# Kernel tuning notes

Hardware: AMD Instinct MI355X
Metric: run time of the kernel (lower is better)

## Reference

```python
import jax, jax.numpy as jnp
import numpy as np

D = 4096      # hidden_size
H = 32        # num_attention_heads
DH = 128      # head_dim
DR = 64       # rope_head_dim (rotated suffix of head_dim)
G = 4         # o_groups
QLR = 1536    # q_lora_rank
OLR = 512     # o_lora_rank
WIN = 2048    # window_size
EPS = 1e-6    # norm_eps
THETA = 10000.0


def rms_norm(x, g):
    return x * jax.lax.rsqrt(jnp.mean(x * x, axis=-1, keepdims=True) + EPS) * g


def rope_interleave(x, cos, sin):
    # interleaved (non-neox) rotary: pairs are adjacent even/odd lanes
    x0, x1 = x[..., 0::2], x[..., 1::2]
    r0 = x0 * cos - x1 * sin
    r1 = x0 * sin + x1 * cos
    return jnp.stack([r0, r1], axis=-1).reshape(x.shape)


def setup_inputs() -> dict:
    ks = jax.random.split(jax.random.key(0), 9)
    B, S = 1, 2048
    return {
        "hidden_states": jax.random.normal(ks[0], (B, S, D), jnp.float32),
        "positions": jnp.arange(S, dtype=jnp.int64),
        "wq_a": jax.random.normal(ks[1], (QLR, D), jnp.float32) * 0.02,
        "q_norm_g": jnp.ones((QLR,), jnp.float32),
        "wq_b": jax.random.normal(ks[2], (H * DH, QLR), jnp.float32) * 0.02,
        "wkv": jax.random.normal(ks[3], (DH, D), jnp.float32) * 0.02,
        "kv_norm_g": jnp.ones((DH,), jnp.float32),
        "wo_a": jax.random.normal(ks[4], (G, OLR, (H * DH) // G), jnp.float32) * 0.02,
        "wo_b": jax.random.normal(ks[5], (D, G * OLR), jnp.float32) * 0.02,
        "attn_sink": jax.random.normal(ks[6], (H,), jnp.float32),
    }


def reference(hidden_states, positions, wq_a, q_norm_g, wq_b, wkv, kv_norm_g, wo_a, wo_b, attn_sink):
    B, S, _ = hidden_states.shape
    # low-rank Q path: wq_a -> RMSNorm -> wq_b -> [B,S,H,DH]
    qr = rms_norm(hidden_states @ wq_a.T, q_norm_g)
    q = (qr @ wq_b.T).reshape(B, S, H, DH)
    # shared latent KV (single head_dim vector, MLA/MQA style): wkv -> RMSNorm
    kv = rms_norm(hidden_states @ wkv.T, kv_norm_g)  # [B,S,DH]
    # rotary tables (interleave mode)
    inv_freq = 1.0 / (THETA ** (jnp.arange(0, DR, 2, dtype=jnp.float32) / DR))
    ang = positions.astype(jnp.float32)[:, None] * inv_freq  # [S, DR/2]
    cos, sin = jnp.cos(ang), jnp.sin(ang)
    # rotate last DR dims of q and k
    q = jnp.concatenate(
        [q[..., : DH - DR], rope_interleave(q[..., DH - DR :], cos[None, :, None, :], sin[None, :, None, :])], -1)
    k = jnp.concatenate(
        [kv[..., : DH - DR], rope_interleave(kv[..., DH - DR :], cos[None, :, :], sin[None, :, :])], -1)
    # windowed causal attention with learned per-head sink logit
    scores = jnp.einsum("bshd,btd->bhst", q, k) * (DH ** -0.5)  # [B,H,S,S]
    i = jnp.arange(S)[:, None]
    j = jnp.arange(S)[None, :]
    mask = (j <= i) & ((i - j) < WIN)
    scores = jnp.where(mask[None, None], scores, jnp.finfo(scores.dtype).min)
    sink = jnp.broadcast_to(attn_sink[None, :, None, None], (B, H, S, 1))
    probs = jax.nn.softmax(jnp.concatenate([scores, sink], axis=-1), axis=-1)[..., :S]
    # value = shared normalized latent (pre-rope)
    out = jnp.einsum("bhst,btd->bshd", probs, kv)  # [B,S,H,DH]
    # grouped low-rank output projection: wo_a per group, then wo_b
    out = out.reshape(B, S, G, (H * DH) // G)
    low = jnp.einsum("bsgd,gkd->bsgk", out, wo_a).reshape(B, S, G * OLR)
    return low @ wo_b.T
```

## Files before the change

### kernel.cpp

```cpp
#include <hip/hip_runtime.h>

typedef unsigned short u16;
typedef __bf16 bf16x8 __attribute__((ext_vector_type(8)));
typedef float  f32x4  __attribute__((ext_vector_type(4)));

#define EPSF 1e-6f

__device__ __forceinline__ u16 f2b(float f) {
  unsigned u = __float_as_uint(f);
  u += 0x7fffu + ((u >> 16) & 1u);
  return (u16)(u >> 16);
}
__device__ __forceinline__ float b2f(u16 u) { return __uint_as_float(((unsigned)u) << 16); }
__device__ __forceinline__ u16 f2bh(float f) { return __builtin_bit_cast(u16, (__bf16)f); }

__device__ __forceinline__ void dma16(const u16* g, u16* l) {
  __builtin_amdgcn_global_load_lds(
      (const __attribute__((address_space(1))) unsigned int*)g,
      (__attribute__((address_space(3))) unsigned int*)l, 16, 0, 0);
}

__global__ void dsv4_cvt(const float* __restrict__ hidden, const float* __restrict__ wq_a,
                         const float* __restrict__ wq_b, const float* __restrict__ wkv,
                         const float* __restrict__ wo_a, const float* __restrict__ wo_b,
                         u16* hb, u16* qab, u16* qbb, u16* kvb, u16* oab, u16* obb)
{
  long c = (long)blockIdx.x * 256 + threadIdx.x;
  const float* s; u16* d; long off;
  if      (c < 1048576) { s = hidden; d = hb;  off = c; }
  else if (c < 1835008) { s = wq_a;   d = qab; off = c - 1048576; }
  else if (c < 2621440) { s = wq_b;   d = qbb; off = c - 1835008; }
  else if (c < 2686976) { s = wkv;    d = kvb; off = c - 2621440; }
  else if (c < 2949120) { s = wo_a;   d = oab; off = c - 2686976; }
  else                  { s = wo_b;   d = obb; off = c - 2949120; }
  const float* p = s + off * 8;
  float4 f0 = *(const float4*)p;
  float4 f1 = *(const float4*)(p + 4);
  union { u16 h[8]; int4 v; } u;
  u.h[0] = f2b(f0.x); u.h[1] = f2b(f0.y); u.h[2] = f2b(f0.z); u.h[3] = f2b(f0.w);
  u.h[4] = f2b(f1.x); u.h[5] = f2b(f1.y); u.h[6] = f2b(f1.z); u.h[7] = f2b(f1.w);
  *(int4*)(d + off * 8) = u.v;
}

template<int BM, bool C_F32>
__global__ __launch_bounds__(256, 2)
void dsv4_gemm(const u16* __restrict__ A, int lda, long sAz,
               const u16* __restrict__ B, int ldb, long sBz,
               void* __restrict__ Cv, int ldc, long sCz,
               int K, int splitTile,
               const u16* __restrict__ Baux, void* __restrict__ Caux, int ldcAux)
{
  constexpr int AJ = BM / 32;
  constexpr int NJ = (BM == 128) ? 4 : 2;
  __shared__ __align__(16) u16 As[2 * BM * 64];
  __shared__ __align__(16) u16 Bs[2 * 128 * 64];

  const int tid   = threadIdx.x;
  const int lane  = tid & 63;
  const int qd    = lane >> 4;
  const int l16   = lane & 15;
  const int wid   = tid >> 6;
  const int wbase = tid & 192;
  const int swz   = l16 & 7;

  int n0 = blockIdx.x * 128;
  const int m0 = blockIdx.y * BM;
  void* Cp = Cv;
  if ((int)blockIdx.x >= splitTile) {
    B = Baux; Cp = Caux; ldc = ldcAux;
    n0 = ((int)blockIdx.x - splitTile) * 128;
  }
  A += (long)blockIdx.z * sAz;
  B += (long)blockIdx.z * sBz;

  const u16* gA[AJ]; u16* lA[AJ];
#pragma unroll
  for (int j = 0; j < AJ; j++) {
    int L = j * 256 + tid, row = L >> 3, c = (L & 7) ^ (row & 7);
    gA[j] = A + (long)(m0 + row) * lda + c * 8;
    lA[j] = As + (j * 256 + wbase) * 8;
  }
  const u16* gB[4]; u16* lB[4];
#pragma unroll
  for (int j = 0; j < 4; j++) {
    int L = j * 256 + tid, row = L >> 3, c = (L & 7) ^ (row & 7);
    gB[j] = B + (long)(n0 + row) * ldb + c * 8;
    lB[j] = Bs + (j * 256 + wbase) * 8;
  }

  f32x4 acc[4][NJ];
#pragma unroll
  for (int i = 0; i < 4; i++)
#pragma unroll
    for (int j = 0; j < NJ; j++) { f32x4 z = {0.f, 0.f, 0.f, 0.f}; acc[i][j] = z; }

  const int wm = (BM == 128) ? (wid >> 1) * 64 : 0;
  const int wn = (BM == 128) ? (wid & 1) * 64 : wid * 32;

  auto issue = [&](int s) {
    const int k  = s << 6;
    const int ab = (s & 1) * (BM * 64);
    const int bb = (s & 1) * (128 * 64);
#pragma unroll
    for (int j = 0; j < AJ; j++) dma16(gA[j] + k, lA[j] + ab);
#pragma unroll
    for (int j = 0; j < 4; j++)  dma16(gB[j] + k, lB[j] + bb);
  };

  const int nsteps = K >> 6;
  issue(0);
  asm volatile("s_waitcnt vmcnt(0)" ::: "memory");
  __builtin_amdgcn_s_barrier();

  for (int t = 0; t < nsteps; t++) {
    if (t + 1 < nsteps) issue(t + 1);
    const int ab = (t & 1) * (BM * 64);
    const int bb = (t & 1) * (128 * 64);

#pragma unroll
    for (int ks2 = 0; ks2 < 2; ks2++) {
      bf16x8 af[4], bg[NJ];
#pragma unroll
      for (int i = 0; i < 4; i++) {
        int row = wm + i * 16 + l16;
        af[i] = *(const bf16x8*)&As[ab + row * 64 + ((((ks2 << 2) + qd) ^ swz) << 3)];
      }
#pragma unroll
      for (int j = 0; j < NJ; j++) {
        int row = wn + j * 16 + l16;
        bg[j] = *(const bf16x8*)&Bs[bb + row * 64 + ((((ks2 << 2) + qd) ^ swz) << 3)];
      }
      __builtin_amdgcn_s_setprio(1);
#pragma unroll
      for (int i = 0; i < 4; i++)
#pragma unroll
        for (int j = 0; j < NJ; j++)
          acc[i][j] = __builtin_amdgcn_mfma_f32_16x16x32_bf16(af[i], bg[j], acc[i][j], 0, 0, 0);
      __builtin_amdgcn_s_setprio(0);
    }

    asm volatile("s_waitcnt lgkmcnt(0)" ::: "memory");
    asm volatile("s_waitcnt vmcnt(0)" ::: "memory");
    __builtin_amdgcn_s_barrier();
  }

#pragma unroll
  for (int i = 0; i < 4; i++)
#pragma unroll
    for (int j = 0; j < NJ; j++)
#pragma unroll
      for (int rr = 0; rr < 4; rr++) {
        long row = m0 + wm + i * 16 + qd * 4 + rr;
        int  col = n0 + wn + j * 16 + l16;
        if (C_F32)
          ((float*)Cp)[row * ldc + col + (long)blockIdx.z * sCz] = acc[i][j][rr];
        else
          ((u16*)Cp)[row * ldc + col + (long)blockIdx.z * sCz] = f2b(acc[i][j][rr]);
      }
}

__global__ void dsv4_rmsnorm(const u16* __restrict__ X, const float* __restrict__ g,
                             u16* __restrict__ Y, int W, float invW)
{
  __shared__ float wsum[4];
  const int row = blockIdx.x;
  const u16* x = X + (long)row * W;
  u16* y = Y + (long)row * W;
  float ss = 0.f;
  for (int i = threadIdx.x; i < W; i += 256) { float v = b2f(x[i]); ss += v * v; }
#pragma unroll
  for (int o = 32; o > 0; o >>= 1) ss += __shfl_xor(ss, o);
  const int wid = threadIdx.x >> 6;
  if ((threadIdx.x & 63) == 0) wsum[wid] = ss;
  __syncthreads();
  float tot = wsum[0] + wsum[1] + wsum[2] + wsum[3];
  float scale = rsqrtf(tot * invW + EPSF);
  for (int i = threadIdx.x; i < W; i += 256)
    y[i] = f2b(b2f(x[i]) * scale * g[i]);
}

__global__ void dsv4_kv_finalize(const u16* __restrict__ KVp, const float* __restrict__ g,
                                 u16* __restrict__ Kout, u16* __restrict__ VTout)
{
  const int wid  = threadIdx.x >> 6;
  const int lane = threadIdx.x & 63;
  const int row  = blockIdx.x * 4 + wid;
  const u16* x = KVp + (long)row * 128;
  float x0 = b2f(x[2 * lane]);
  float x1 = b2f(x[2 * lane + 1]);
  float ss = x0 * x0 + x1 * x1;
#pragma unroll
  for (int o = 32; o > 0; o >>= 1) ss += __shfl_xor(ss, o);
  float scale = rsqrtf(ss * (1.f / 128.f) + EPSF);
  float v0 = x0 * scale * g[2 * lane];
  float v1 = x1 * scale * g[2 * lane + 1];
  VTout[(long)(2 * lane) * 2048 + row]     = f2b(v0);
  VTout[(long)(2 * lane + 1) * 2048 + row] = f2b(v1);
  float k0 = v0, k1 = v1;
  if (lane >= 32) {
    int i = lane - 32;
    float invf = powf(10000.f, -(float)i * (1.f / 32.f));
    float sn, cc;
    sincosf((float)row * invf, &sn, &cc);
    k0 = v0 * cc - v1 * sn;
    k1 = v0 * sn + v1 * cc;
  }
  Kout[(long)row * 128 + 2 * lane]     = f2b(k0);
  Kout[(long)row * 128 + 2 * lane + 1] = f2b(k1);
}

__device__ __forceinline__ void attn_step(
    const bf16x8* qf, bool diag, const u16* __restrict__ KsB,
    const u16* __restrict__ VsB, u16* __restrict__ PsW,
    int w, int qd, int l16, int swz, float* m, float* negm, float* l, f32x4* o)
{
  const float scl2 = 0.12754245006257017f;
  const float THRU = 62.0f;
  f32x4 st[4];
#pragma unroll
  for (int i = 0; i < 4; i++) { f32x4 z = {0.f, 0.f, 0.f, 0.f}; st[i] = z; }

  __builtin_amdgcn_s_setprio(1);
#pragma unroll
  for (int ks = 0; ks < 4; ks++) {
#pragma unroll
    for (int nt = 0; nt < 4; nt++) {
      int row = nt * 16 + l16;
      bf16x8 bk = *(const bf16x8*)&KsB[row * 128 + ((((ks << 2) + qd) ^ swz) << 3)];
      st[nt] = __builtin_amdgcn_mfma_f32_16x16x32_bf16(qf[ks], bk, st[nt], 0, 0, 0);
    }
  }
  __builtin_amdgcn_s_setprio(0);

  if (diag) {
#pragma unroll
    for (int nt = 0; nt < 4; nt++)
#pragma unroll
      for (int rr = 0; rr < 4; rr++)
        if ((nt * 16 + l16) > (w * 16 + qd * 4 + rr)) st[nt][rr] = -3.0e38f;
  }

  float tm[4];
  bool need = false;
#pragma unroll
  for (int rr = 0; rr < 4; rr++) {
    float t = fmaxf(fmaxf(st[0][rr], st[1][rr]), fmaxf(st[2][rr], st[3][rr]));
    t = fmaxf(t, __shfl_xor(t, 1));
    t = fmaxf(t, __shfl_xor(t, 2));
    t = fmaxf(t, __shfl_xor(t, 4));
    t = fmaxf(t, __shfl_xor(t, 8));
    tm[rr] = t;
    need = need || (t > m[rr] + THRU);
  }
  if (__any(need)) {
#pragma unroll
    for (int rr = 0; rr < 4; rr++) {
      float mn = fmaxf(m[rr], tm[rr]);
      float a  = exp2f(scl2 * (m[rr] - mn));
      m[rr] = mn; negm[rr] = -scl2 * mn;
      l[rr] *= a;
#pragma unroll
      for (int nt = 0; nt < 8; nt++) o[nt][rr] *= a;
    }
  }

#pragma unroll
  for (int nt = 0; nt < 4; nt++)
#pragma unroll
    for (int rr = 0; rr < 4; rr++) {
      float p = exp2f(fmaf(st[nt][rr], scl2, negm[rr]));
      l[rr] += p;
      int row = qd * 4 + rr;
      int cl2 = ((nt << 1) + (l16 >> 3)) ^ (row & 7);
      PsW[row * 64 + (cl2 << 3) + (l16 & 7)] = f2bh(p);
    }
  asm volatile("s_waitcnt lgkmcnt(0)" ::: "memory");

  __builtin_amdgcn_s_setprio(1);
#pragma unroll
  for (int ks = 0; ks < 2; ks++) {
    bf16x8 ap = *(const bf16x8*)&PsW[l16 * 64 + ((((ks << 2) + qd) ^ swz) << 3)];
#pragma unroll
    for (int nt = 0; nt < 8; nt++) {
      int row = nt * 16 + l16;
      bf16x8 bv = *(const bf16x8*)&VsB[row * 64 + ((((ks << 2) + qd) ^ swz) << 3)];
      o[nt] = __builtin_amdgcn_mfma_f32_16x16x32_bf16(ap, bv, o[nt], 0, 0, 0);
    }
  }
  __builtin_amdgcn_s_setprio(0);
}

__global__ __launch_bounds__(256, 2)
void dsv4_attn(const u16* __restrict__ Q, const u16* __restrict__ Km,
               const u16* __restrict__ VT, const float* __restrict__ sinkp,
               u16* __restrict__ O)
{
  __shared__ __align__(16) u16 Ks[2][64 * 128];
  __shared__ __align__(16) u16 Vs[2][128 * 64];
  __shared__ __align__(16) u16 Ps[4][16 * 64];

  const int b  = blockIdx.x;
  const int h  = blockIdx.y;
  const int qtA = 31 - b, qtB = b;
  const int n1 = qtA + 1, nT = n1 + qtB + 1;
  const int tid  = threadIdx.x;
  const int lane = tid & 63;
  const int w    = tid >> 6;
  const int qd   = lane >> 4;
  const int l16  = lane & 15;
  const int swz  = l16 & 7;

  bf16x8 qfA[4], qfB[4];
#pragma unroll
  for (int t = 0; t < 2; t++) {
    int srow = (t ? qtB : qtA) * 64 + w * 16 + l16;
    const u16* qp = Q + (long)srow * 4096 + h * 128 + qd * 8;
    bf16x8* qf = t ? qfB : qfA;
#pragma unroll
    for (int ks = 0; ks < 4; ks++) {
      union { int4 v; u16 hh[8]; } u;
      u.v = *(const int4*)(qp + ks * 32);
      if (ks >= 2) {
#pragma unroll
        for (int j = 0; j < 4; j++) {
          int i = (ks - 2) * 16 + qd * 4 + j;
          float invf = exp2f((float)i * (-13.287712379549449f / 32.f));
          float sn, cc;
          sincosf((float)srow * invf, &sn, &cc);
          float x0 = b2f(u.hh[2 * j]), x1 = b2f(u.hh[2 * j + 1]);
          u.hh[2 * j]     = f2b(x0 * cc - x1 * sn);
          u.hh[2 * j + 1] = f2b(x0 * sn + x1 * cc);
        }
      }
      qf[ks] = *(bf16x8*)&u;
    }
  }

  const u16* gK[4]; const u16* gV[4]; int lKo[4], lVo[4];
#pragma unroll
  for (int j = 0; j < 4; j++) {
    int cl = j * 256 + tid;
    int krow = cl >> 4, kc = (cl & 15) ^ (krow & 7);
    gK[j] = Km + (long)krow * 128 + kc * 8;
    lKo[j] = (j * 256 + (tid & 192)) * 8;
    int vrow = cl >> 3, vc = (cl & 7) ^ (vrow & 7);
    gV[j] = VT + (long)vrow * 2048 + vc * 8;
    lVo[j] = (j * 256 + (tid & 192)) * 8;
  }

  float m[4], negm[4], l[4];
  f32x4 o[8];
#pragma unroll
  for (int i = 0; i < 4; i++) { m[i] = -INFINITY; negm[i] = 0.f; l[i] = 0.f; }
#pragma unroll
  for (int i = 0; i < 8; i++) { f32x4 z = {0.f, 0.f, 0.f, 0.f}; o[i] = z; }

  const float sink2 = sinkp[h] * 1.4426950408889634f;

#pragma unroll
  for (int j = 0; j < 4; j++) { dma16(gK[j], &Ks[0][lKo[j]]); dma16(gV[j], &Vs[0][lVo[j]]); }

  for (int it = 0; it < nT; ++it) {
    int nxt = it + 1;
    if (nxt < nT) {
      int kt2 = (nxt < n1) ? nxt : nxt - n1;
      int pb = nxt & 1;
#pragma unroll
      for (int j = 0; j < 4; j++) {
        dma16(gK[j] + (long)kt2 * 8192, &Ks[pb][lKo[j]]);
        dma16(gV[j] + (long)kt2 * 64,   &Vs[pb][lVo[j]]);
      }
    }
    asm volatile("s_waitcnt vmcnt(8)" ::: "memory");
    asm volatile("s_barrier" ::: "memory");
    const int cb = it & 1;

    if (it < n1)
      attn_step(qfA, it == n1 - 1, Ks[cb], Vs[cb], Ps[w], w, qd, l16, swz, m, negm, l, o);
    else
      attn_step(qfB, it == nT - 1, Ks[cb], Vs[cb], Ps[w], w, qd, l16, swz, m, negm, l, o);

    asm volatile("s_barrier" ::: "memory");

    if (it == n1 - 1) {
      float inv[4];
#pragma unroll
      for (int rr = 0; rr < 4; rr++) {
        float ls = l[rr];
        ls += __shfl_xor(ls, 1);
        ls += __shfl_xor(ls, 2);
        ls += __shfl_xor(ls, 4);
        ls += __shfl_xor(ls, 8);
        inv[rr] = 1.f / (ls + exp2f(sink2 + negm[rr]));
      }
#pragma unroll
      for (int nt = 0; nt < 8; nt++)
#pragma unroll
        for (int rr = 0; rr < 4; rr++)
          O[(long)(qtA * 64 + w * 16 + qd * 4 + rr) * 4096 + h * 128 + nt * 16 + l16] =
              f2bh(o[nt][rr] * inv[rr]);
#pragma unroll
      for (int i = 0; i < 4; i++) { m[i] = -INFINITY; negm[i] = 0.f; l[i] = 0.f; }
#pragma unroll
      for (int i = 0; i < 8; i++) { f32x4 z = {0.f, 0.f, 0.f, 0.f}; o[i] = z; }
    }
  }

  float inv[4];
#pragma unroll
  for (int rr = 0; rr < 4; rr++) {
    float ls = l[rr];
    ls += __shfl_xor(ls, 1);
    ls += __shfl_xor(ls, 2);
    ls += __shfl_xor(ls, 4);
    ls += __shfl_xor(ls, 8);
    inv[rr] = 1.f / (ls + exp2f(sink2 + negm[rr]));
  }
#pragma unroll
  for (int nt = 0; nt < 8; nt++)
#pragma unroll
    for (int rr = 0; rr < 4; rr++)
      O[(long)(qtB * 64 + w * 16 + qd * 4 + rr) * 4096 + h * 128 + nt * 16 + l16] =
          f2bh(o[nt][rr] * inv[rr]);
}

extern "C" void kernel_launch(void* const* d_in, const int* in_sizes, int n_in,
                              void* d_out, int out_size, void* d_ws, size_t ws_size,
                              hipStream_t stream)
{
  (void)in_sizes; (void)n_in; (void)out_size; (void)ws_size;
  const float* hidden = (const float*)d_in[0];
  const float* wq_a  = (const float*)d_in[2];
  const float* q_g   = (const float*)d_in[3];
  const float* wq_b  = (const float*)d_in[4];
  const float* wkv   = (const float*)d_in[5];
  const float* kv_g  = (const float*)d_in[6];
  const float* wo_a  = (const float*)d_in[7];
  const float* wo_b  = (const float*)d_in[8];
  const float* sinkp = (const float*)d_in[9];
  float* out = (float*)d_out;

  char* ws = (char*)d_ws;
  u16* hb     = (u16*)(ws);
  u16* low    = (u16*)(ws);
  u16* qab    = (u16*)(ws + (17ul << 20));
  u16* qr     = (u16*)(ws + (17ul << 20));
  u16* qbb    = (u16*)(ws + (30ul << 20));
  u16* kvb    = (u16*)(ws + (43ul << 20));
  u16* oab    = (u16*)(ws + (45ul << 20));
  u16* obb    = (u16*)(ws + (50ul << 20));
  u16* qbuf   = (u16*)(ws + (67ul << 20));
  u16* attnout= (u16*)(ws + (84ul << 20));
  u16* qr_pre = (u16*)(ws + (101ul << 20));
  u16* kvpre  = (u16*)(ws + (108ul << 20));
  u16* kmat   = (u16*)(ws + (108ul << 20) + 524288u);
  u16* vt     = (u16*)(ws + (108ul << 20) + 1048576u);

  const int BIG = 1 << 29;
  dim3 blk(256);

  dsv4_cvt<<<15616, blk, 0, stream>>>(hidden, wq_a, wq_b, wkv, wo_a, wo_b,
                                      hb, qab, qbb, kvb, oab, obb);
  dsv4_gemm<64, false><<<dim3(13, 32, 1), blk, 0, stream>>>(
      hb, 4096, 0, qab, 4096, 0, qr_pre, 1536, 0, 4096, 12, kvb, kvpre, 128);
  dsv4_rmsnorm<<<2048, blk, 0, stream>>>(qr_pre, q_g, qr, 1536, 1.f / 1536.f);
  dsv4_kv_finalize<<<512, blk, 0, stream>>>(kvpre, kv_g, kmat, vt);
  dsv4_gemm<128, false><<<dim3(32, 16, 1), blk, 0, stream>>>(
      qr, 1536, 0, qbb, 1536, 0, qbuf, 4096, 0, 1536, BIG, nullptr, nullptr, 0);
  dsv4_attn<<<dim3(16, 32, 1), blk, 0, stream>>>(qbuf, kmat, vt, sinkp, attnout);
  dsv4_gemm<64, false><<<dim3(4, 32, 4), blk, 0, stream>>>(
      attnout, 4096, 1024, oab, 1024, 524288, low, 2048, 512, 1024, BIG,
      nullptr, nullptr, 0);
  dsv4_gemm<128, true><<<dim3(32, 16, 1), blk, 0, stream>>>(
      low, 2048, 0, obb, 2048, 0, out, 4096, 0, 2048, BIG, nullptr, nullptr, 0);
}
```

Before: 403.1 us.

## Compute transposed QK^T scores and pass P to PV MFMA in registers

```diff
diff --git a/kernel.cpp b/kernel.cpp
--- a/kernel.cpp
+++ b/kernel.cpp
@@ -13,6 +13,12 @@
 }
 __device__ __forceinline__ float b2f(u16 u) { return __uint_as_float(((unsigned)u) << 16); }
 __device__ __forceinline__ u16 f2bh(float f) { return __builtin_bit_cast(u16, (__bf16)f); }
+
+__device__ __forceinline__ unsigned cvtpk(float lo, float hi) {
+  unsigned d;
+  asm("v_cvt_pk_bf16_f32 %0, %1, %2" : "=v"(d) : "v"(lo), "v"(hi));
+  return d;
+}
 
 __device__ __forceinline__ void dma16(const u16* g, u16* l) {
   __builtin_amdgcn_global_load_lds(
@@ -211,8 +217,8 @@
 
 __device__ __forceinline__ void attn_step(
     const bf16x8* qf, bool diag, const u16* __restrict__ KsB,
-    const u16* __restrict__ VsB, u16* __restrict__ PsW,
-    int w, int qd, int l16, int swz, float* m, float* negm, float* l, f32x4* o)
+    const u16* __restrict__ VsB,
+    int w, int qd, int l16, int swz, float& m, float& negm, float& l, f32x4* o)
 {
   const float scl2 = 0.12754245006257017f;
   const float THRU = 62.0f;
@@ -227,7 +233,7 @@
     for (int nt = 0; nt < 4; nt++) {
       int row = nt * 16 + l16;
       bf16x8 bk = *(const bf16x8*)&KsB[row * 128 + ((((ks << 2) + qd) ^ swz) << 3)];
-      st[nt] = __builtin_amdgcn_mfma_f32_16x16x32_bf16(qf[ks], bk, st[nt], 0, 0, 0);
+      st[nt] = __builtin_amdgcn_mfma_f32_16x16x32_bf16(bk, qf[ks], st[nt], 0, 0, 0);
     }
   }
   __builtin_amdgcn_s_setprio(0);
@@ -237,54 +243,58 @@
     for (int nt = 0; nt < 4; nt++)
 #pragma unroll
       for (int rr = 0; rr < 4; rr++)
-        if ((nt * 16 + l16) > (w * 16 + qd * 4 + rr)) st[nt][rr] = -3.0e38f;
-  }
-
-  float tm[4];
-  bool need = false;
-#pragma unroll
-  for (int rr = 0; rr < 4; rr++) {
-    float t = fmaxf(fmaxf(st[0][rr], st[1][rr]), fmaxf(st[2][rr], st[3][rr]));
-    t = fmaxf(t, __shfl_xor(t, 1));
-    t = fmaxf(t, __shfl_xor(t, 2));
-    t = fmaxf(t, __shfl_xor(t, 4));
-    t = fmaxf(t, __shfl_xor(t, 8));
-    tm[rr] = t;
-    need = need || (t > m[rr] + THRU);
-  }
-  if (__any(need)) {
+        if ((nt * 16 + qd * 4 + rr) > (w * 16 + l16)) st[nt][rr] = -3.0e38f;
+  }
+
+  float t0 = fmaxf(fmaxf(st[0][0], st[0][1]), fmaxf(st[0][2], st[0][3]));
+  float t1 = fmaxf(fmaxf(st[1][0], st[1][1]), fmaxf(st[1][2], st[1][3]));
+  float t2 = fmaxf(fmaxf(st[2][0], st[2][1]), fmaxf(st[2][2], st[2][3]));
+  float t3 = fmaxf(fmaxf(st[3][0], st[3][1]), fmaxf(st[3][2], st[3][3]));
+  float t = fmaxf(fmaxf(t0, t1), fmaxf(t2, t3));
+  t = fmaxf(t, __shfl_xor(t, 16));
+  t = fmaxf(t, __shfl_xor(t, 32));
+
+  if (__any(t > m + THRU)) {
+    float mn = fmaxf(m, t);
+    float aq = exp2f(scl2 * (m - mn));
+    m = mn; negm = -scl2 * mn;
+    l *= aq;
+    float a4[4];
+#pragma unroll
+    for (int rr = 0; rr < 4; rr++) a4[rr] = __shfl(aq, qd * 4 + rr);
+#pragma unroll
+    for (int nt = 0; nt < 8; nt++)
+#pragma unroll
+      for (int rr = 0; rr < 4; rr++) o[nt][rr] *= a4[rr];
+  }
+
+#pragma unroll
+  for (int nt = 0; nt < 4; nt++)
 #pragma unroll
     for (int rr = 0; rr < 4; rr++) {
-      float mn = fmaxf(m[rr], tm[rr]);
-      float a  = exp2f(scl2 * (m[rr] - mn));
-      m[rr] = mn; negm[rr] = -scl2 * mn;
-      l[rr] *= a;
-#pragma unroll
-      for (int nt = 0; nt < 8; nt++) o[nt][rr] *= a;
-    }
-  }
-
-#pragma unroll
-  for (int nt = 0; nt < 4; nt++)
-#pragma unroll
-    for (int rr = 0; rr < 4; rr++) {
-      float p = exp2f(fmaf(st[nt][rr], scl2, negm[rr]));
-      l[rr] += p;
-      int row = qd * 4 + rr;
-      int cl2 = ((nt << 1) + (l16 >> 3)) ^ (row & 7);
-      PsW[row * 64 + (cl2 << 3) + (l16 & 7)] = f2bh(p);
-    }
-  asm volatile("s_waitcnt lgkmcnt(0)" ::: "memory");
+      float p = exp2f(fmaf(st[nt][rr], scl2, negm));
+      l += p;
+      st[nt][rr] = p;
+    }
 
   __builtin_amdgcn_s_setprio(1);
 #pragma unroll
   for (int ks = 0; ks < 2; ks++) {
-    bf16x8 ap = *(const bf16x8*)&PsW[l16 * 64 + ((((ks << 2) + qd) ^ swz) << 3)];
+    unsigned A0 = cvtpk(st[2 * ks][0],     st[2 * ks][1]);
+    unsigned A1 = cvtpk(st[2 * ks][2],     st[2 * ks][3]);
+    unsigned B0 = cvtpk(st[2 * ks + 1][0], st[2 * ks + 1][1]);
+    unsigned B1 = cvtpk(st[2 * ks + 1][2], st[2 * ks + 1][3]);
+    auto s0 = __builtin_amdgcn_permlane32_swap(A0, B0, false, false);
+    auto u0 = __builtin_amdgcn_permlane16_swap(s0[0], s0[1], false, false);
+    auto s1 = __builtin_amdgcn_permlane32_swap(A1, B1, false, false);
+    auto u1 = __builtin_amdgcn_permlane16_swap(s1[0], s1[1], false, false);
+    union { unsigned d[4]; bf16x8 v; } ap;
+    ap.d[0] = u0[0]; ap.d[1] = u1[0]; ap.d[2] = u0[1]; ap.d[3] = u1[1];
 #pragma unroll
     for (int nt = 0; nt < 8; nt++) {
       int row = nt * 16 + l16;
       bf16x8 bv = *(const bf16x8*)&VsB[row * 64 + ((((ks << 2) + qd) ^ swz) << 3)];
-      o[nt] = __builtin_amdgcn_mfma_f32_16x16x32_bf16(ap, bv, o[nt], 0, 0, 0);
+      o[nt] = __builtin_amdgcn_mfma_f32_16x16x32_bf16(ap.v, bv, o[nt], 0, 0, 0);
     }
   }
   __builtin_amdgcn_s_setprio(0);
@@ -297,7 +307,6 @@
 {
   __shared__ __align__(16) u16 Ks[2][64 * 128];
   __shared__ __align__(16) u16 Vs[2][128 * 64];
-  __shared__ __align__(16) u16 Ps[4][16 * 64];
 
   const int b  = blockIdx.x;
   const int h  = blockIdx.y;
@@ -348,10 +357,8 @@
     lVo[j] = (j * 256 + (tid & 192)) * 8;
   }
 
-  float m[4], negm[4], l[4];
+  float m = -INFINITY, negm = 0.f, l = 0.f;
   f32x4 o[8];
-#pragma unroll
-  for (int i = 0; i < 4; i++) { m[i] = -INFINITY; negm[i] = 0.f; l[i] = 0.f; }
 #pragma unroll
   for (int i = 0; i < 8; i++) { f32x4 z = {0.f, 0.f, 0.f, 0.f}; o[i] = z; }
 
@@ -376,52 +383,47 @@
     const int cb = it & 1;
 
     if (it < n1)
-      attn_step(qfA, it == n1 - 1, Ks[cb], Vs[cb], Ps[w], w, qd, l16, swz, m, negm, l, o);
+      attn_step(qfA, it == n1 - 1, Ks[cb], Vs[cb], w, qd, l16, swz, m, negm, l, o);
     else
-      attn_step(qfB, it == nT - 1, Ks[cb], Vs[cb], Ps[w], w, qd, l16, swz, m, negm, l, o);
+      attn_step(qfB, it == nT - 1, Ks[cb], Vs[cb], w, qd, l16, swz, m, negm, l, o);
 
     asm volatile("s_barrier" ::: "memory");
 
     if (it == n1 - 1) {
-      float inv[4];
-#pragma unroll
-      for (int rr = 0; rr < 4; rr++) {
-        float ls = l[rr];
-        ls += __shfl_xor(ls, 1);
-        ls += __shfl_xor(ls, 2);
-        ls += __shfl_xor(ls, 4);
-        ls += __shfl_xor(ls, 8);
-        inv[rr] = 1.f / (ls + exp2f(sink2 + negm[rr]));
-      }
+      float ls = l;
+      ls += __shfl_xor(ls, 16);
+      ls += __shfl_xor(ls, 32);
+      float inv = 1.f / (ls + exp2f(sink2 + negm));
+      float inv4[4];
+#pragma unroll
+      for (int rr = 0; rr < 4; rr++) inv4[rr] = __shfl(inv, qd * 4 + rr);
 #pragma unroll
       for (int nt = 0; nt < 8; nt++)
 #pragma unroll
         for (int rr = 0; rr < 4; rr++)
           O[(long)(qtA * 64 + w * 16 + qd * 4 + rr) * 4096 + h * 128 + nt * 16 + l16] =
-              f2bh(o[nt][rr] * inv[rr]);
-#pragma unroll
-      for (int i = 0; i < 4; i++) { m[i] = -INFINITY; negm[i] = 0.f; l[i] = 0.f; }
+              f2bh(o[nt][rr] * inv4[rr]);
+      m = -INFINITY; negm = 0.f; l = 0.f;
 #pragma unroll
       for (int i = 0; i < 8; i++) { f32x4 z = {0.f, 0.f, 0.f, 0.f}; o[i] = z; }
     }
   }
 
-  float inv[4];
-#pragma unroll
-  for (int rr = 0; rr < 4; rr++) {
-    float ls = l[rr];
-    ls += __shfl_xor(ls, 1);
-    ls += __shfl_xor(ls, 2);
-    ls += __shfl_xor(ls, 4);
-    ls += __shfl_xor(ls, 8);
-    inv[rr] = 1.f / (ls + exp2f(sink2 + negm[rr]));
-  }
-#pragma unroll
-  for (int nt = 0; nt < 8; nt++)
-#pragma unroll
-    for (int rr = 0; rr < 4; rr++)
-      O[(long)(qtB * 64 + w * 16 + qd * 4 + rr) * 4096 + h * 128 + nt * 16 + l16] =
-          f2bh(o[nt][rr] * inv[rr]);
+  {
+    float ls = l;
+    ls += __shfl_xor(ls, 16);
+    ls += __shfl_xor(ls, 32);
+    float inv = 1.f / (ls + exp2f(sink2 + negm));
+    float inv4[4];
+#pragma unroll
+    for (int rr = 0; rr < 4; rr++) inv4[rr] = __shfl(inv, qd * 4 + rr);
+#pragma unroll
+    for (int nt = 0; nt < 8; nt++)
+#pragma unroll
+      for (int rr = 0; rr < 4; rr++)
+        O[(long)(qtB * 64 + w * 16 + qd * 4 + rr) * 4096 + h * 128 + nt * 16 + l16] =
+            f2bh(o[nt][rr] * inv4[rr]);
+  }
 }
 
 extern "C" void kernel_launch(void* const* d_in, const int* in_sizes, int n_in,
```

New measurement: 386.7 us. 1.04x faster.
